# Kernel tuning notes

Measured on AMD Instinct MI355X. Metric: run time of the kernel, lower is better.

Reference implementation:

```python
import jax, jax.numpy as jnp
import numpy as np

EMB = 512
HEADS = 8
KEY_DIM = 64


def setup_inputs() -> dict:
    key = jax.random.key(0)
    k1, k2, k3, k4, k5 = jax.random.split(key, 5)
    B, S = 4, 2048
    x = jax.random.normal(k1, (B, S, EMB), dtype=jnp.float32)
    keys = jax.random.normal(k2, (B, HEADS, S, KEY_DIM), dtype=jnp.float32)
    values = jax.random.normal(k3, (B, HEADS, S, KEY_DIM), dtype=jnp.float32)
    # torch.rand -> uniform [0,1)
    query_weights = jax.random.uniform(k4, (EMB, KEY_DIM * HEADS), dtype=jnp.float32)
    output_weights = jax.random.uniform(k5, (KEY_DIM * HEADS, EMB), dtype=jnp.float32)
    return {"x": x, "keys": keys, "values": values,
            "query_weights": query_weights, "output_weights": output_weights}


def reference(x, keys, values, query_weights, output_weights):
    B, S, _ = x.shape
    # Q projection: [B,S,E] @ [E,H*K] -> [B,H,S,K]
    q = (x @ query_weights).reshape(B, S, HEADS, KEY_DIM).transpose(0, 2, 1, 3)
    # scores: [B,H,S,S]
    scores = jnp.einsum('bhqk,bhsk->bhqs', q, keys) / jnp.sqrt(jnp.float32(KEY_DIM))
    attn = jax.nn.softmax(scores, axis=-1)
    # context: [B,H,S,K] -> [B,S,H*K]
    ctx = jnp.einsum('bhqs,bhsk->bhqk', attn, values)
    ctx = ctx.transpose(0, 2, 1, 3).reshape(B, S, HEADS * KEY_DIM)
    return ctx @ output_weights
```

## Files before the change

kernel.cpp:

```cpp
#include <hip/hip_runtime.h>
#include <hip/hip_bf16.h>

#define EMB 512
#define HEADS 8
#define KD 64
#define SEQ 2048
#define BATCH 4

typedef __attribute__((ext_vector_type(8))) short bf16x8;
typedef __attribute__((ext_vector_type(4))) float f32x4;

__device__ __forceinline__ unsigned short f2bf(float x) {
    union { float f; unsigned u; } v; v.f = x;
    unsigned r = v.u + 0x7fff + ((v.u >> 16) & 1);
    return (unsigned short)(r >> 16);
}
__device__ __forceinline__ float bf2f(unsigned short b) {
    union { unsigned u; float f; } v; v.u = ((unsigned)b) << 16;
    return v.f;
}
__device__ __forceinline__ unsigned pk2(float a, float b) {
    __hip_bfloat162 h = __float22bfloat162_rn(float2{a, b});
    unsigned u; __builtin_memcpy(&u, &h, 4); return u;
}

__global__ __launch_bounds__(256) void prep_all_kernel(
    const float* __restrict__ x,  const float* __restrict__ wq,
    const float* __restrict__ wo, const float* __restrict__ K,
    const float* __restrict__ V,
    unsigned short* __restrict__ ximg, unsigned short* __restrict__ wqimg,
    unsigned short* __restrict__ woimg, unsigned short* __restrict__ kimg,
    unsigned short* __restrict__ vimg) {
    const int bid = blockIdx.x;
    const int t   = threadIdx.x;

    if (bid < 1024) {
        const int rb = bid >> 3, ch = bid & 7;
        const float* src = x + (size_t)rb * 64 * EMB + ch * 64;
        unsigned short* dhi = ximg + (size_t)bid * 8192;
        unsigned short* dlo = dhi + 4096;
#pragma unroll
        for (int it = 0; it < 4; ++it) {
            const int idx = t + it * 256;
            const int row = idx >> 4, c4 = (idx & 15) << 2;
            const float4 v = *(const float4*)(src + (size_t)row * EMB + c4);
            const unsigned short h0 = f2bf(v.x), h1 = f2bf(v.y),
                                 h2 = f2bf(v.z), h3 = f2bf(v.w);
            *(uint2*)&dhi[row * 64 + c4] = make_uint2(
                (unsigned)h0 | ((unsigned)h1 << 16),
                (unsigned)h2 | ((unsigned)h3 << 16));
            *(uint2*)&dlo[row * 64 + c4] = make_uint2(
                (unsigned)f2bf(v.x - bf2f(h0)) | ((unsigned)f2bf(v.y - bf2f(h1)) << 16),
                (unsigned)f2bf(v.z - bf2f(h2)) | ((unsigned)f2bf(v.w - bf2f(h3)) << 16));
        }
    } else if (bid < 1152) {
        int widx = bid - 1024;
        const bool isq = widx < 64;
        if (!isq) widx -= 64;
        const int nb = widx >> 3, ch = widx & 7;
        const float* src = (isq ? wq : wo) + (size_t)(ch * 64) * EMB + nb * 64;
        unsigned short* dhi = isq ? (wqimg + (size_t)widx * 8192)
                                  : (woimg + (size_t)widx * 4096);
        unsigned short* dlo = dhi + 4096;
#pragma unroll
        for (int it = 0; it < 2; ++it) {
            const int idx = t + it * 256;
            const int sp  = idx & 31;
            const int c4  = (idx >> 5) << 2;
            const float* r0 = src + (size_t)(2 * sp) * EMB + c4;
            const float4 a = *(const float4*)r0;
            const float4 b = *(const float4*)(r0 + EMB);
#pragma unroll
            for (int j = 0; j < 4; ++j) {
                const float aj = (&a.x)[j], bj = (&b.x)[j];
                const unsigned short ah = f2bf(aj), bh = f2bf(bj);
                *(unsigned*)&dhi[(c4 + j) * 64 + 2 * sp] =
                    (unsigned)ah | ((unsigned)bh << 16);
                if (isq)
                    *(unsigned*)&dlo[(c4 + j) * 64 + 2 * sp] =
                        (unsigned)f2bf(aj - bf2f(ah)) | ((unsigned)f2bf(bj - bf2f(bh)) << 16);
            }
        }
    } else if (bid < 2176) {
        const int kt = bid - 1152;
        const float4* src = (const float4*)(K + (size_t)kt * 4096);
        unsigned short* dhi = kimg + (size_t)kt * 8192;
        unsigned short* dlo = dhi + 4096;
#pragma unroll
        for (int it = 0; it < 4; ++it) {
            const int idx = t + it * 256;
            const float4 v = src[idx];
            const unsigned short h0 = f2bf(v.x), h1 = f2bf(v.y),
                                 h2 = f2bf(v.z), h3 = f2bf(v.w);
            *(uint2*)&dhi[idx * 4] = make_uint2(
                (unsigned)h0 | ((unsigned)h1 << 16),
                (unsigned)h2 | ((unsigned)h3 << 16));
            *(uint2*)&dlo[idx * 4] = make_uint2(
                (unsigned)f2bf(v.x - bf2f(h0)) | ((unsigned)f2bf(v.y - bf2f(h1)) << 16),
                (unsigned)f2bf(v.z - bf2f(h2)) | ((unsigned)f2bf(v.w - bf2f(h3)) << 16));
        }
    } else {
        const int vt = bid - 2176;
        const float* src = V + (size_t)vt * 4096;
        unsigned short* dst = vimg + (size_t)vt * 4096;
#pragma unroll
        for (int it = 0; it < 2; ++it) {
            const int idx = t + it * 256;
            const int sp  = idx & 31;
            const int d4  = (idx >> 5) << 2;
            const float4 a = *(const float4*)(src + (2 * sp) * KD + d4);
            const float4 b = *(const float4*)(src + (2 * sp + 1) * KD + d4);
#pragma unroll
            for (int j = 0; j < 4; ++j) {
                *(unsigned*)&dst[(d4 + j) * 64 + 2 * sp] =
                    (unsigned)f2bf((&a.x)[j]) | ((unsigned)f2bf((&b.x)[j]) << 16);
            }
        }
    }
}

__global__ __launch_bounds__(256) void proj_q_kernel(
    const unsigned short* __restrict__ ximg,
    const unsigned short* __restrict__ wqimg,
    unsigned short* __restrict__ qhi_img,
    unsigned short* __restrict__ qlo_img) {
    __shared__ unsigned short x_s[2][64][72];
    __shared__ unsigned short w_t[2][64][72];

    const int t  = threadIdx.x;
    const int w  = t >> 6;
    const int l  = t & 63;
    const int g  = l >> 4;
    const int ln = l & 15;

    const int rb = blockIdx.x;
    const int nb = blockIdx.y;

    f32x4 acc[4];
#pragma unroll
    for (int cb = 0; cb < 4; ++cb) acc[cb] = (f32x4){0.f, 0.f, 0.f, 0.f};

    for (int ch = 0; ch < 8; ++ch) {
        __syncthreads();
        const uint4* xs = (const uint4*)(ximg + (size_t)(rb * 8 + ch) * 8192);
        const uint4* ws = (const uint4*)(wqimg + (size_t)(nb * 8 + ch) * 8192);
#pragma unroll
        for (int it = 0; it < 4; ++it) {
            const int idx = t + it * 256;
            const int hl  = idx >> 9;
            const int rem = idx & 511;
            *(uint4*)&x_s[hl][rem >> 3][(rem & 7) * 8] = xs[idx];
            *(uint4*)&w_t[hl][rem >> 3][(rem & 7) * 8] = ws[idx];
        }
        __syncthreads();

        bf16x8 ah[2], al[2];
#pragma unroll
        for (int kk = 0; kk < 2; ++kk) {
            ah[kk] = *(const bf16x8*)&x_s[0][w * 16 + ln][g * 8 + 32 * kk];
            al[kk] = *(const bf16x8*)&x_s[1][w * 16 + ln][g * 8 + 32 * kk];
        }
#pragma unroll
        for (int cb = 0; cb < 4; ++cb) {
            f32x4 c = acc[cb];
#pragma unroll
            for (int kk = 0; kk < 2; ++kk) {
                const bf16x8 bh = *(const bf16x8*)&w_t[0][cb * 16 + ln][g * 8 + 32 * kk];
                const bf16x8 bl = *(const bf16x8*)&w_t[1][cb * 16 + ln][g * 8 + 32 * kk];
                c = __builtin_amdgcn_mfma_f32_16x16x32_bf16(al[kk], bh, c, 0, 0, 0);
                c = __builtin_amdgcn_mfma_f32_16x16x32_bf16(ah[kk], bl, c, 0, 0, 0);
                c = __builtin_amdgcn_mfma_f32_16x16x32_bf16(ah[kk], bh, c, 0, 0, 0);
            }
            acc[cb] = c;
        }
    }

#pragma unroll
    for (int cb = 0; cb < 4; ++cb) {
#pragma unroll
        for (int r = 0; r < 4; ++r) {
            const int row = rb * 64 + w * 16 + 4 * g + r;
            const int k   = cb * 16 + ln;
            const float v = acc[cb][r] * 0.125f;
            const unsigned short hi = f2bf(v);
            const unsigned short lo = f2bf(v - bf2f(hi));
            const size_t off = ((size_t)((row >> 11) * HEADS + nb) * SEQ + (row & 2047)) * KD + k;
            qhi_img[off] = hi;
            qlo_img[off] = lo;
        }
    }
}

__global__ __launch_bounds__(256) void proj_o_kernel(
    const unsigned short* __restrict__ ctximg,
    const unsigned short* __restrict__ woimg,
    float* __restrict__ out) {
    __shared__ unsigned short x_s[64][72];
    __shared__ unsigned short w_t[64][72];

    const int t  = threadIdx.x;
    const int w  = t >> 6;
    const int l  = t & 63;
    const int g  = l >> 4;
    const int ln = l & 15;

    const int rb = blockIdx.x;
    const int nb = blockIdx.y;

    f32x4 acc[4];
#pragma unroll
    for (int cb = 0; cb < 4; ++cb) acc[cb] = (f32x4){0.f, 0.f, 0.f, 0.f};

    for (int ch = 0; ch < 8; ++ch) {
        __syncthreads();
        const uint4* xs = (const uint4*)(ctximg + (size_t)(rb * 8 + ch) * 4096);
        const uint4* ws = (const uint4*)(woimg + (size_t)(nb * 8 + ch) * 4096);
#pragma unroll
        for (int it = 0; it < 2; ++it) {
            const int idx = t + it * 256;
            *(uint4*)&x_s[idx >> 3][(idx & 7) * 8] = xs[idx];
            *(uint4*)&w_t[idx >> 3][(idx & 7) * 8] = ws[idx];
        }
        __syncthreads();

        bf16x8 ah[2];
#pragma unroll
        for (int kk = 0; kk < 2; ++kk)
            ah[kk] = *(const bf16x8*)&x_s[w * 16 + ln][g * 8 + 32 * kk];
#pragma unroll
        for (int cb = 0; cb < 4; ++cb) {
            f32x4 c = acc[cb];
#pragma unroll
            for (int kk = 0; kk < 2; ++kk) {
                const bf16x8 bh = *(const bf16x8*)&w_t[cb * 16 + ln][g * 8 + 32 * kk];
                c = __builtin_amdgcn_mfma_f32_16x16x32_bf16(ah[kk], bh, c, 0, 0, 0);
            }
            acc[cb] = c;
        }
    }

#pragma unroll
    for (int cb = 0; cb < 4; ++cb) {
#pragma unroll
        for (int r = 0; r < 4; ++r) {
            const int row = rb * 64 + w * 16 + 4 * g + r;
            const int col = nb * 64 + cb * 16 + ln;
            out[(size_t)row * EMB + col] = acc[cb][r];
        }
    }
}

__global__ __launch_bounds__(256) void attn4_kernel(
    const unsigned short* __restrict__ qhi_img,
    const unsigned short* __restrict__ qlo_img,
    const unsigned short* __restrict__ kimg,
    const unsigned short* __restrict__ vimg,
    unsigned short* __restrict__ ctximg) {
    constexpr int NT  = 64;
    constexpr int LDK = 72;

    __shared__ unsigned short k_s[2][NT][LDK];
    __shared__ unsigned short v_t[KD][LDK];
    __shared__ unsigned short p_s[4][16][LDK];

    const int t  = threadIdx.x;
    const int w  = t >> 6;
    const int l  = t & 63;
    const int g  = l >> 4;
    const int ln = l & 15;

    const int bh = blockIdx.y;
    const int q0 = blockIdx.x * 64 + w * 16;

    bf16x8 qhi[2], qlo[2];
    {
        const size_t qoff = ((size_t)bh * SEQ + q0 + ln) * KD;
#pragma unroll
        for (int kk = 0; kk < 2; ++kk) {
            qhi[kk] = *(const bf16x8*)&qhi_img[qoff + g * 8 + 32 * kk];
            qlo[kk] = *(const bf16x8*)&qlo_img[qoff + g * 8 + 32 * kk];
        }
    }

    f32x4 acc[4];
#pragma unroll
    for (int db = 0; db < 4; ++db) acc[db] = (f32x4){0.f, 0.f, 0.f, 0.f};
    float m_run = -1e30f, l_run = 0.0f;

    for (int tile = 0; tile < SEQ / NT; ++tile) {
        __syncthreads();

        const uint4* ksrc = (const uint4*)(kimg + (size_t)(bh * 32 + tile) * 8192);
#pragma unroll
        for (int it = 0; it < 4; ++it) {
            const int idx = t + it * 256;
            const int hl  = idx >> 9;
            const int rem = idx & 511;
            *(uint4*)&k_s[hl][rem >> 3][(rem & 7) * 8] = ksrc[idx];
        }
        const uint4* vsrc = (const uint4*)(vimg + (size_t)(bh * 32 + tile) * 4096);
#pragma unroll
        for (int it = 0; it < 2; ++it) {
            const int idx = t + it * 256;
            *(uint4*)&v_t[idx >> 3][(idx & 7) * 8] = vsrc[idx];
        }
        __syncthreads();

        f32x4 st[4];
#pragma unroll
        for (int sb = 0; sb < 4; ++sb) {
            f32x4 c = (f32x4){0.f, 0.f, 0.f, 0.f};
#pragma unroll
            for (int kk = 0; kk < 2; ++kk) {
                const bf16x8 khi = *(const bf16x8*)&k_s[0][sb * 16 + ln][g * 8 + 32 * kk];
                const bf16x8 klo = *(const bf16x8*)&k_s[1][sb * 16 + ln][g * 8 + 32 * kk];
                c = __builtin_amdgcn_mfma_f32_16x16x32_bf16(klo, qhi[kk], c, 0, 0, 0);
                c = __builtin_amdgcn_mfma_f32_16x16x32_bf16(khi, qlo[kk], c, 0, 0, 0);
                c = __builtin_amdgcn_mfma_f32_16x16x32_bf16(khi, qhi[kk], c, 0, 0, 0);
            }
            st[sb] = c;
        }

        float tm = st[0][0];
#pragma unroll
        for (int sb = 0; sb < 4; ++sb)
#pragma unroll
            for (int r = 0; r < 4; ++r) tm = fmaxf(tm, st[sb][r]);
        tm = fmaxf(tm, __shfl_xor(tm, 16));
        tm = fmaxf(tm, __shfl_xor(tm, 32));

        const float m_new  = fmaxf(m_run, tm);
        const float scalef = __expf(m_run - m_new);
        m_run = m_new;

        float rs = 0.f;
#pragma unroll
        for (int sb = 0; sb < 4; ++sb) {
            const float p0 = __expf(st[sb][0] - m_new);
            const float p1 = __expf(st[sb][1] - m_new);
            const float p2 = __expf(st[sb][2] - m_new);
            const float p3 = __expf(st[sb][3] - m_new);
            rs += (p0 + p1) + (p2 + p3);
            *(uint2*)&p_s[w][ln][sb * 16 + g * 4] =
                make_uint2(pk2(p0, p1), pk2(p2, p3));
        }
        rs += __shfl_xor(rs, 16);
        rs += __shfl_xor(rs, 32);
        l_run = l_run * scalef + rs;

#pragma unroll
        for (int r = 0; r < 4; ++r) {
            const float sr = __shfl(scalef, 4 * g + r);
#pragma unroll
            for (int db = 0; db < 4; ++db) acc[db][r] *= sr;
        }

        bf16x8 pa[2];
#pragma unroll
        for (int kk = 0; kk < 2; ++kk)
            pa[kk] = *(const bf16x8*)&p_s[w][ln][g * 8 + 32 * kk];
#pragma unroll
        for (int db = 0; db < 4; ++db) {
            f32x4 c = acc[db];
#pragma unroll
            for (int kk = 0; kk < 2; ++kk) {
                const bf16x8 vb = *(const bf16x8*)&v_t[ln + 16 * db][g * 8 + 32 * kk];
                c = __builtin_amdgcn_mfma_f32_16x16x32_bf16(pa[kk], vb, c, 0, 0, 0);
            }
            acc[db] = c;
        }
    }

    const float invl = 1.0f / l_run;
    const int rb  = (bh >> 3) * 32 + blockIdx.x;
    const int chh = bh & 7;
    unsigned short* cbase = ctximg + ((size_t)rb * 8 + chh) * 4096;
#pragma unroll
    for (int r = 0; r < 4; ++r) {
        const float iv = __shfl(invl, 4 * g + r);
        const int row = w * 16 + 4 * g + r;
#pragma unroll
        for (int db = 0; db < 4; ++db)
            cbase[row * 64 + db * 16 + ln] = f2bf(acc[db][r] * iv);
    }
}

__global__ __launch_bounds__(256) void prep_k_kernel(const float* __restrict__ K,
                                                     unsigned short* __restrict__ kimg) {
    const int bt = blockIdx.x;
    const float4* src = (const float4*)(K + (size_t)bt * 4096);
    unsigned short* dhi = kimg + (size_t)bt * 8192;
    unsigned short* dlo = dhi + 4096;
#pragma unroll
    for (int it = 0; it < 4; ++it) {
        const int idx = threadIdx.x + it * 256;
        const float4 v = src[idx];
        const unsigned short h0 = f2bf(v.x), h1 = f2bf(v.y),
                             h2 = f2bf(v.z), h3 = f2bf(v.w);
        *(uint2*)&dhi[idx * 4] = make_uint2(
            (unsigned)h0 | ((unsigned)h1 << 16),
            (unsigned)h2 | ((unsigned)h3 << 16));
        *(uint2*)&dlo[idx * 4] = make_uint2(
            (unsigned)f2bf(v.x - bf2f(h0)) | ((unsigned)f2bf(v.y - bf2f(h1)) << 16),
            (unsigned)f2bf(v.z - bf2f(h2)) | ((unsigned)f2bf(v.w - bf2f(h3)) << 16));
    }
}

__global__ __launch_bounds__(256) void prep_v_kernel(const float* __restrict__ V,
                                                     unsigned short* __restrict__ vimg) {
    const int bt = blockIdx.x;
    const float* src = V + (size_t)bt * 4096;
    unsigned short* dst = vimg + (size_t)bt * 4096;
#pragma unroll
    for (int it = 0; it < 2; ++it) {
        const int idx = threadIdx.x + it * 256;
        const int sp  = idx & 31;
        const int d4  = (idx >> 5) << 2;
        const float4 a = *(const float4*)(src + (2 * sp) * KD + d4);
        const float4 b = *(const float4*)(src + (2 * sp + 1) * KD + d4);
#pragma unroll
        for (int j = 0; j < 4; ++j) {
            *(unsigned*)&dst[(d4 + j) * 64 + 2 * sp] =
                (unsigned)f2bf((&a.x)[j]) | ((unsigned)f2bf((&b.x)[j]) << 16);
        }
    }
}

template <int PREP>
__global__ __launch_bounds__(256) void attn3_kernel(const float* __restrict__ Q,
                                                    const float* __restrict__ Keys,
                                                    const float* __restrict__ Vals,
                                                    const unsigned short* __restrict__ kimg,
                                                    const unsigned short* __restrict__ vimg,
                                                    float* __restrict__ out) {
    constexpr int NT  = 64;
    constexpr int LDK = 72;

    __shared__ unsigned short k_s[2][NT][LDK];
    __shared__ unsigned short v_t[KD][LDK];
    __shared__ unsigned short p_s[4][16][LDK];

    const int t  = threadIdx.x;
    const int w  = t >> 6;
    const int l  = t & 63;
    const int g  = l >> 4;
    const int ln = l & 15;

    const int bh = blockIdx.y;
    const int q0 = blockIdx.x * 64 + w * 16;

    const float* kbase = Keys + (size_t)bh * SEQ * KD;
    const float* vbase = Vals + (size_t)bh * SEQ * KD;
    const float* qptr  = Q + ((size_t)bh * SEQ + q0 + ln) * KD;

    bf16x8 qhi[2], qlo[2];
#pragma unroll
    for (int kk = 0; kk < 2; ++kk) {
        const float* p = qptr + g * 8 + 32 * kk;
#pragma unroll
        for (int j = 0; j < 8; ++j) {
            const float xv = p[j] * 0.125f;
            const unsigned short h = f2bf(xv);
            qhi[kk][j] = (short)h;
            qlo[kk][j] = (short)f2bf(xv - bf2f(h));
        }
    }

    f32x4 acc[4];
#pragma unroll
    for (int db = 0; db < 4; ++db) acc[db] = (f32x4){0.f, 0.f, 0.f, 0.f};
    float m_run = -1e30f, l_run = 0.0f;

    for (int tile = 0; tile < SEQ / NT; ++tile) {
        __syncthreads();

        if (PREP) {
            const uint4* ksrc = (const uint4*)(kimg + (size_t)(bh * 32 + tile) * 8192);
#pragma unroll
            for (int it = 0; it < 4; ++it) {
                const int idx = t + it * 256;
                const int hl  = idx >> 9;
                const int rem = idx & 511;
                *(uint4*)&k_s[hl][rem >> 3][(rem & 7) * 8] = ksrc[idx];
            }
            const uint4* vsrc = (const uint4*)(vimg + (size_t)(bh * 32 + tile) * 4096);
#pragma unroll
            for (int it = 0; it < 2; ++it) {
                const int idx = t + it * 256;
                *(uint4*)&v_t[idx >> 3][(idx & 7) * 8] = vsrc[idx];
            }
        } else {
            const float* kt = kbase + (size_t)tile * NT * KD;
            const float* vt = vbase + (size_t)tile * NT * KD;
#pragma unroll
            for (int it = 0; it < 4; ++it) {
                const int idx = t + it * 256;
                const int s   = idx >> 4;
                const int d4  = (idx & 15) << 2;
                const float4 kv = *(const float4*)(kt + s * KD + d4);
                unsigned short h0 = f2bf(kv.x), h1 = f2bf(kv.y),
                               h2 = f2bf(kv.z), h3 = f2bf(kv.w);
                *(uint2*)&k_s[0][s][d4] = make_uint2(
                    (unsigned)h0 | ((unsigned)h1 << 16),
                    (unsigned)h2 | ((unsigned)h3 << 16));
                *(uint2*)&k_s[1][s][d4] = make_uint2(
                    (unsigned)f2bf(kv.x - bf2f(h0)) | ((unsigned)f2bf(kv.y - bf2f(h1)) << 16),
                    (unsigned)f2bf(kv.z - bf2f(h2)) | ((unsigned)f2bf(kv.w - bf2f(h3)) << 16));
            }
#pragma unroll
            for (int it = 0; it < 2; ++it) {
                const int idx = t + it * 256;
                const int sp  = idx & 31;
                const int d4  = (idx >> 5) << 2;
                const float* v0 = vt + (2 * sp) * KD + d4;
                const float4 a = *(const float4*)v0;
                const float4 b = *(const float4*)(v0 + KD);
#pragma unroll
                for (int j = 0; j < 4; ++j) {
                    *(unsigned*)&v_t[d4 + j][2 * sp] =
                        (unsigned)f2bf((&a.x)[j]) | ((unsigned)f2bf((&b.x)[j]) << 16);
                }
            }
        }
        __syncthreads();

        f32x4 st[4];
#pragma unroll
        for (int sb = 0; sb < 4; ++sb) {
            f32x4 c = (f32x4){0.f, 0.f, 0.f, 0.f};
#pragma unroll
            for (int kk = 0; kk < 2; ++kk) {
                const bf16x8 khi = *(const bf16x8*)&k_s[0][sb * 16 + ln][g * 8 + 32 * kk];
                const bf16x8 klo = *(const bf16x8*)&k_s[1][sb * 16 + ln][g * 8 + 32 * kk];
                c = __builtin_amdgcn_mfma_f32_16x16x32_bf16(klo, qhi[kk], c, 0, 0, 0);
                c = __builtin_amdgcn_mfma_f32_16x16x32_bf16(khi, qlo[kk], c, 0, 0, 0);
                c = __builtin_amdgcn_mfma_f32_16x16x32_bf16(khi, qhi[kk], c, 0, 0, 0);
            }
            st[sb] = c;
        }

        float tm = st[0][0];
#pragma unroll
        for (int sb = 0; sb < 4; ++sb)
#pragma unroll
            for (int r = 0; r < 4; ++r) tm = fmaxf(tm, st[sb][r]);
        tm = fmaxf(tm, __shfl_xor(tm, 16));
        tm = fmaxf(tm, __shfl_xor(tm, 32));

        const float m_new  = fmaxf(m_run, tm);
        const float scalef = __expf(m_run - m_new);
        m_run = m_new;

        float rs = 0.f;
#pragma unroll
        for (int sb = 0; sb < 4; ++sb) {
            const float p0 = __expf(st[sb][0] - m_new);
            const float p1 = __expf(st[sb][1] - m_new);
            const float p2 = __expf(st[sb][2] - m_new);
            const float p3 = __expf(st[sb][3] - m_new);
            rs += (p0 + p1) + (p2 + p3);
            *(uint2*)&p_s[w][ln][sb * 16 + g * 4] =
                make_uint2(pk2(p0, p1), pk2(p2, p3));
        }
        rs += __shfl_xor(rs, 16);
        rs += __shfl_xor(rs, 32);
        l_run = l_run * scalef + rs;

#pragma unroll
        for (int r = 0; r < 4; ++r) {
            const float sr = __shfl(scalef, 4 * g + r);
#pragma unroll
            for (int db = 0; db < 4; ++db) acc[db][r] *= sr;
        }

        bf16x8 pa[2];
#pragma unroll
        for (int kk = 0; kk < 2; ++kk)
            pa[kk] = *(const bf16x8*)&p_s[w][ln][g * 8 + 32 * kk];
#pragma unroll
        for (int db = 0; db < 4; ++db) {
            f32x4 c = acc[db];
#pragma unroll
            for (int kk = 0; kk < 2; ++kk) {
                const bf16x8 vb = *(const bf16x8*)&v_t[ln + 16 * db][g * 8 + 32 * kk];
                c = __builtin_amdgcn_mfma_f32_16x16x32_bf16(pa[kk], vb, c, 0, 0, 0);
            }
            acc[db] = c;
        }
    }

    const float invl = 1.0f / l_run;
    const int b = bh >> 3, h = bh & 7;
#pragma unroll
    for (int r = 0; r < 4; ++r) {
        const float iv = __shfl(invl, 4 * g + r);
        float* orow = out + ((size_t)(b * SEQ + q0 + 4 * g + r) * EMB) + h * KD + ln;
#pragma unroll
        for (int db = 0; db < 4; ++db) orow[16 * db] = acc[db][r] * iv;
    }
}

template <int TRANSQ>
__global__ __launch_bounds__(256) void proj_mfma_kernel(const float* __restrict__ in,
                                                        const float* __restrict__ W,
                                                        float* __restrict__ out) {
    __shared__ unsigned short x_s[2][64][72];
    __shared__ unsigned short w_t[2][64][72];

    const int t  = threadIdx.x;
    const int w  = t >> 6;
    const int l  = t & 63;
    const int g  = l >> 4;
    const int ln = l & 15;

    const int row0 = blockIdx.x * 64;
    const int n0   = blockIdx.y * 64;

    f32x4 acc[4];
#pragma unroll
    for (int cb = 0; cb < 4; ++cb) acc[cb] = (f32x4){0.f, 0.f, 0.f, 0.f};

    for (int ch = 0; ch < EMB / 64; ++ch) {
        __syncthreads();
#pragma unroll
        for (int it = 0; it < 4; ++it) {
            const int idx = t + it * 256;
            const int s   = idx >> 4;
            const int d4  = (idx & 15) << 2;
            const float4 xv = *(const float4*)(in + (size_t)(row0 + s) * EMB + ch * 64 + d4);
            const unsigned short h0 = f2bf(xv.x), h1 = f2bf(xv.y),
                                 h2 = f2bf(xv.z), h3 = f2bf(xv.w);
            *(uint2*)&x_s[0][s][d4] = make_uint2(
                (unsigned)h0 | ((unsigned)h1 << 16),
                (unsigned)h2 | ((unsigned)h3 << 16));
            *(uint2*)&x_s[1][s][d4] = make_uint2(
                (unsigned)f2bf(xv.x - bf2f(h0)) | ((unsigned)f2bf(xv.y - bf2f(h1)) << 16),
                (unsigned)f2bf(xv.z - bf2f(h2)) | ((unsigned)f2bf(xv.w - bf2f(h3)) << 16));
        }
#pragma unroll
        for (int it = 0; it < 2; ++it) {
            const int idx = t + it * 256;
            const int sp  = idx & 31;
            const int c4  = (idx >> 5) << 2;
            const float* wrow = W + (size_t)(ch * 64 + 2 * sp) * EMB + n0 + c4;
            const float4 a = *(const float4*)wrow;
            const float4 b = *(const float4*)(wrow + EMB);
#pragma unroll
            for (int j = 0; j < 4; ++j) {
                const float aj = (&a.x)[j], bj = (&b.x)[j];
                const unsigned short ah = f2bf(aj), bh = f2bf(bj);
                *(unsigned*)&w_t[0][c4 + j][2 * sp] =
                    (unsigned)ah | ((unsigned)bh << 16);
                *(unsigned*)&w_t[1][c4 + j][2 * sp] =
                    (unsigned)f2bf(aj - bf2f(ah)) | ((unsigned)f2bf(bj - bf2f(bh)) << 16);
            }
        }
        __syncthreads();

        bf16x8 ah[2], al[2];
#pragma unroll
        for (int kk = 0; kk < 2; ++kk) {
            ah[kk] = *(const bf16x8*)&x_s[0][w * 16 + ln][g * 8 + 32 * kk];
            al[kk] = *(const bf16x8*)&x_s[1][w * 16 + ln][g * 8 + 32 * kk];
        }
#pragma unroll
        for (int cb = 0; cb < 4; ++cb) {
            f32x4 c = acc[cb];
#pragma unroll
            for (int kk = 0; kk < 2; ++kk) {
                const bf16x8 bh = *(const bf16x8*)&w_t[0][cb * 16 + ln][g * 8 + 32 * kk];
                const bf16x8 bl = *(const bf16x8*)&w_t[1][cb * 16 + ln][g * 8 + 32 * kk];
                c = __builtin_amdgcn_mfma_f32_16x16x32_bf16(al[kk], bh, c, 0, 0, 0);
                c = __builtin_amdgcn_mfma_f32_16x16x32_bf16(ah[kk], bl, c, 0, 0, 0);
                c = __builtin_amdgcn_mfma_f32_16x16x32_bf16(ah[kk], bh, c, 0, 0, 0);
            }
            acc[cb] = c;
        }
    }

#pragma unroll
    for (int cb = 0; cb < 4; ++cb) {
#pragma unroll
        for (int r = 0; r < 4; ++r) {
            const int row = row0 + w * 16 + 4 * g + r;
            const int col = n0 + cb * 16 + ln;
            if (TRANSQ) {
                const int b = row >> 11, s = row & 2047;
                const int h = col >> 6, k = col & 63;
                out[((size_t)(b * HEADS + h) * SEQ + s) * KD + k] = acc[cb][r];
            } else {
                out[(size_t)row * EMB + col] = acc[cb][r];
            }
        }
    }
}

__global__ __launch_bounds__(256) void proj_fp32_kernel(const float* __restrict__ in,
                                                        const float* __restrict__ W,
                                                        float* __restrict__ out) {
    __shared__ float x_s[8][EMB];
    const int block_row = blockIdx.x * 8;

    const float4* in4 = (const float4*)(in + (size_t)block_row * EMB);
    float4* xs4 = (float4*)(&x_s[0][0]);
    for (int i = threadIdx.x; i < 8 * EMB / 4; i += 256) xs4[i] = in4[i];
    __syncthreads();

    const int n  = (threadIdx.x & 127) * 4;
    const int rg = threadIdx.x >> 7;

    float acc[4][4] = {};
    for (int e = 0; e < EMB; ++e) {
        const float4 w4 = *(const float4*)(W + (size_t)e * EMB + n);
#pragma unroll
        for (int rr = 0; rr < 4; ++rr) {
            const float xv = x_s[rg + rr * 2][e];
            acc[rr][0] += xv * w4.x;
            acc[rr][1] += xv * w4.y;
            acc[rr][2] += xv * w4.z;
            acc[rr][3] += xv * w4.w;
        }
    }
#pragma unroll
    for (int rr = 0; rr < 4; ++rr) {
        const int row = block_row + rg + rr * 2;
        float4 o;
        o.x = acc[rr][0]; o.y = acc[rr][1]; o.z = acc[rr][2]; o.w = acc[rr][3];
        *(float4*)(out + (size_t)row * EMB + n) = o;
    }
}

extern "C" void kernel_launch(void* const* d_in, const int* in_sizes, int n_in,
                              void* d_out, int out_size, void* d_ws, size_t ws_size,
                              hipStream_t stream) {
    const float* x  = (const float*)d_in[0];
    const float* ks = (const float*)d_in[1];
    const float* vs = (const float*)d_in[2];
    const float* wq = (const float*)d_in[3];
    const float* wo = (const float*)d_in[4];
    float* out = (float*)d_out;

    const int M = BATCH * SEQ;

    const size_t XIMG_OFF = 0;
    const size_t WQ_OFF   = 16777216;
    const size_t WO_OFF   = 17825792;
    const size_t KIMG_OFF = 18350080;
    const size_t VIMG_OFF = 35127296;
    const size_t QHI_OFF  = 43515904;
    const size_t QLO_OFF  = 51904512;
    const size_t CTX_OFF  = 60293120;
    const size_t TIER_A   = 68681728;

    if (ws_size >= TIER_A) {
        unsigned short* ximg  = (unsigned short*)((char*)d_ws + XIMG_OFF);
        unsigned short* wqimg = (unsigned short*)((char*)d_ws + WQ_OFF);
        unsigned short* woimg = (unsigned short*)((char*)d_ws + WO_OFF);
        unsigned short* kimg  = (unsigned short*)((char*)d_ws + KIMG_OFF);
        unsigned short* vimg  = (unsigned short*)((char*)d_ws + VIMG_OFF);
        unsigned short* qhi   = (unsigned short*)((char*)d_ws + QHI_OFF);
        unsigned short* qlo   = (unsigned short*)((char*)d_ws + QLO_OFF);
        unsigned short* ctx   = (unsigned short*)((char*)d_ws + CTX_OFF);

        prep_all_kernel<<<dim3(3200), dim3(256), 0, stream>>>(
            x, wq, wo, ks, vs, ximg, wqimg, woimg, kimg, vimg);
        proj_q_kernel<<<dim3(M / 64, HEADS), dim3(256), 0, stream>>>(ximg, wqimg, qhi, qlo);
        attn4_kernel<<<dim3(SEQ / 64, BATCH * HEADS), dim3(256), 0, stream>>>(
            qhi, qlo, kimg, vimg, ctx);
        proj_o_kernel<<<dim3(M / 64, EMB / 64), dim3(256), 0, stream>>>(ctx, woimg, out);
        return;
    }

    const size_t QBYTES  = (size_t)BATCH * HEADS * SEQ * KD * 4;
    const size_t CBYTES  = (size_t)BATCH * SEQ * EMB * 4;
    const size_t KIBYTES = (size_t)BATCH * HEADS * SEQ * KD * 2 * 2;
    const size_t VIBYTES = (size_t)BATCH * HEADS * SEQ * KD * 2;

    float* Q = (float*)d_ws;
    const bool mid_ws  = ws_size >= QBYTES + CBYTES;
    const bool full_ws = ws_size >= QBYTES + CBYTES + KIBYTES + VIBYTES;
    float* ctxf = mid_ws ? (float*)((char*)d_ws + QBYTES) : out;
    unsigned short* kimg = (unsigned short*)((char*)d_ws + QBYTES + CBYTES);
    unsigned short* vimg = (unsigned short*)((char*)d_ws + QBYTES + CBYTES + KIBYTES);

    proj_mfma_kernel<1><<<dim3(M / 64, EMB / 64), dim3(256), 0, stream>>>(x, wq, Q);

    if (full_ws) {
        prep_k_kernel<<<dim3(BATCH * HEADS * 32), dim3(256), 0, stream>>>(ks, kimg);
        prep_v_kernel<<<dim3(BATCH * HEADS * 32), dim3(256), 0, stream>>>(vs, vimg);
        attn3_kernel<1><<<dim3(SEQ / 64, BATCH * HEADS), dim3(256), 0, stream>>>(
            Q, ks, vs, kimg, vimg, ctxf);
    } else {
        attn3_kernel<0><<<dim3(SEQ / 64, BATCH * HEADS), dim3(256), 0, stream>>>(
            Q, ks, vs, nullptr, nullptr, ctxf);
    }

    if (mid_ws) {
        proj_mfma_kernel<0><<<dim3(M / 64, EMB / 64), dim3(256), 0, stream>>>(ctxf, wo, out);
    } else {
        proj_fp32_kernel<<<dim3(M / 8), dim3(256), 0, stream>>>(ctxf, wo, out);
    }
}
```

Measured before the change: 245.3 us.

## Rewrite attention with 32x32 MFMA tiles, split-KV waves, and lazy rescaling

```diff
diff --git a/kernel.cpp b/kernel.cpp
--- a/kernel.cpp
+++ b/kernel.cpp
@@ -9,6 +9,7 @@
 
 typedef __attribute__((ext_vector_type(8))) short bf16x8;
 typedef __attribute__((ext_vector_type(4))) float f32x4;
+typedef __attribute__((ext_vector_type(16))) float f32x16;
 
 __device__ __forceinline__ unsigned short f2bf(float x) {
     union { float f; unsigned u; } v; v.f = x;
@@ -250,44 +251,47 @@
     }
 }
 
-__global__ __launch_bounds__(256) void attn4_kernel(
+__global__ __launch_bounds__(256) void attn5_kernel(
     const unsigned short* __restrict__ qhi_img,
     const unsigned short* __restrict__ qlo_img,
     const unsigned short* __restrict__ kimg,
     const unsigned short* __restrict__ vimg,
     unsigned short* __restrict__ ctximg) {
-    constexpr int NT  = 64;
     constexpr int LDK = 72;
-
-    __shared__ unsigned short k_s[2][NT][LDK];
-    __shared__ unsigned short v_t[KD][LDK];
-    __shared__ unsigned short p_s[4][16][LDK];
-
-    const int t  = threadIdx.x;
-    const int w  = t >> 6;
-    const int l  = t & 63;
-    const int g  = l >> 4;
-    const int ln = l & 15;
+    constexpr int LDP = 40;
+
+    __shared__ unsigned short k_s[2][64][LDK];
+    __shared__ unsigned short v_t[64][LDK];
+    __shared__ unsigned short p_s[4][32][LDP];
+    __shared__ float m_arr[2][2][32], l_arr[2][2][32];
+
+    const int t   = threadIdx.x;
+    const int w   = t >> 6;
+    const int l   = t & 63;
+    const int qh  = w >> 1;
+    const int sh  = w & 1;
+    const int q32 = l & 31;
+    const int h   = l >> 5;
 
     const int bh = blockIdx.y;
-    const int q0 = blockIdx.x * 64 + w * 16;
-
-    bf16x8 qhi[2], qlo[2];
+    const int q0 = blockIdx.x * 64;
+
+    bf16x8 qhi[4], qlo[4];
     {
-        const size_t qoff = ((size_t)bh * SEQ + q0 + ln) * KD;
-#pragma unroll
-        for (int kk = 0; kk < 2; ++kk) {
-            qhi[kk] = *(const bf16x8*)&qhi_img[qoff + g * 8 + 32 * kk];
-            qlo[kk] = *(const bf16x8*)&qlo_img[qoff + g * 8 + 32 * kk];
-        }
-    }
-
-    f32x4 acc[4];
-#pragma unroll
-    for (int db = 0; db < 4; ++db) acc[db] = (f32x4){0.f, 0.f, 0.f, 0.f};
-    float m_run = -1e30f, l_run = 0.0f;
-
-    for (int tile = 0; tile < SEQ / NT; ++tile) {
+        const size_t qoff = ((size_t)bh * SEQ + q0 + qh * 32 + q32) * KD + 8 * h;
+#pragma unroll
+        for (int ks = 0; ks < 4; ++ks) {
+            qhi[ks] = *(const bf16x8*)&qhi_img[qoff + 16 * ks];
+            qlo[ks] = *(const bf16x8*)&qlo_img[qoff + 16 * ks];
+        }
+    }
+
+    f32x16 acc0, acc1;
+#pragma unroll
+    for (int i = 0; i < 16; ++i) { acc0[i] = 0.f; acc1[i] = 0.f; }
+    float m_run = -1e30f, l_run = 0.f;
+
+    for (int tile = 0; tile < SEQ / 64; ++tile) {
         __syncthreads();
 
         const uint4* ksrc = (const uint4*)(kimg + (size_t)(bh * 32 + tile) * 8192);
@@ -306,82 +310,93 @@
         }
         __syncthreads();
 
-        f32x4 st[4];
-#pragma unroll
-        for (int sb = 0; sb < 4; ++sb) {
-            f32x4 c = (f32x4){0.f, 0.f, 0.f, 0.f};
-#pragma unroll
-            for (int kk = 0; kk < 2; ++kk) {
-                const bf16x8 khi = *(const bf16x8*)&k_s[0][sb * 16 + ln][g * 8 + 32 * kk];
-                const bf16x8 klo = *(const bf16x8*)&k_s[1][sb * 16 + ln][g * 8 + 32 * kk];
-                c = __builtin_amdgcn_mfma_f32_16x16x32_bf16(klo, qhi[kk], c, 0, 0, 0);
-                c = __builtin_amdgcn_mfma_f32_16x16x32_bf16(khi, qlo[kk], c, 0, 0, 0);
-                c = __builtin_amdgcn_mfma_f32_16x16x32_bf16(khi, qhi[kk], c, 0, 0, 0);
-            }
-            st[sb] = c;
-        }
-
-        float tm = st[0][0];
-#pragma unroll
-        for (int sb = 0; sb < 4; ++sb)
-#pragma unroll
-            for (int r = 0; r < 4; ++r) tm = fmaxf(tm, st[sb][r]);
-        tm = fmaxf(tm, __shfl_xor(tm, 16));
+        f32x16 st;
+#pragma unroll
+        for (int i = 0; i < 16; ++i) st[i] = 0.f;
+        const int srow = sh * 32 + q32;
+#pragma unroll
+        for (int ks = 0; ks < 4; ++ks) {
+            const bf16x8 khi = *(const bf16x8*)&k_s[0][srow][16 * ks + 8 * h];
+            const bf16x8 klo = *(const bf16x8*)&k_s[1][srow][16 * ks + 8 * h];
+            st = __builtin_amdgcn_mfma_f32_32x32x16_bf16(klo, qhi[ks], st, 0, 0, 0);
+            st = __builtin_amdgcn_mfma_f32_32x32x16_bf16(khi, qlo[ks], st, 0, 0, 0);
+            st = __builtin_amdgcn_mfma_f32_32x32x16_bf16(khi, qhi[ks], st, 0, 0, 0);
+        }
+
+        float tm = st[0];
+#pragma unroll
+        for (int i = 1; i < 16; ++i) tm = fmaxf(tm, st[i]);
         tm = fmaxf(tm, __shfl_xor(tm, 32));
 
-        const float m_new  = fmaxf(m_run, tm);
-        const float scalef = __expf(m_run - m_new);
-        m_run = m_new;
+        if (__any(tm > m_run + 8.0f)) {
+            const float m_new = fmaxf(m_run, tm);
+            const float sc = __expf(m_run - m_new);
+            m_run = m_new;
+            l_run *= sc;
+#pragma unroll
+            for (int r = 0; r < 16; ++r) {
+                const int qrow = (r & 3) + 8 * (r >> 2) + 4 * h;
+                const float sr = __shfl(sc, qrow);
+                acc0[r] *= sr; acc1[r] *= sr;
+            }
+        }
 
         float rs = 0.f;
 #pragma unroll
-        for (int sb = 0; sb < 4; ++sb) {
-            const float p0 = __expf(st[sb][0] - m_new);
-            const float p1 = __expf(st[sb][1] - m_new);
-            const float p2 = __expf(st[sb][2] - m_new);
-            const float p3 = __expf(st[sb][3] - m_new);
-            rs += (p0 + p1) + (p2 + p3);
-            *(uint2*)&p_s[w][ln][sb * 16 + g * 4] =
-                make_uint2(pk2(p0, p1), pk2(p2, p3));
-        }
-        rs += __shfl_xor(rs, 16);
+        for (int i = 0; i < 8; ++i) {
+            const float pa_ = __expf(st[2 * i]     - m_run);
+            const float pb_ = __expf(st[2 * i + 1] - m_run);
+            rs += pa_ + pb_;
+            const int sbase = ((2 * i) & 3) + 8 * (i >> 1) + 4 * h;
+            *(unsigned*)&p_s[w][q32][sbase] = pk2(pa_, pb_);
+        }
         rs += __shfl_xor(rs, 32);
-        l_run = l_run * scalef + rs;
-
-#pragma unroll
-        for (int r = 0; r < 4; ++r) {
-            const float sr = __shfl(scalef, 4 * g + r);
-#pragma unroll
-            for (int db = 0; db < 4; ++db) acc[db][r] *= sr;
-        }
-
-        bf16x8 pa[2];
-#pragma unroll
-        for (int kk = 0; kk < 2; ++kk)
-            pa[kk] = *(const bf16x8*)&p_s[w][ln][g * 8 + 32 * kk];
-#pragma unroll
-        for (int db = 0; db < 4; ++db) {
-            f32x4 c = acc[db];
-#pragma unroll
-            for (int kk = 0; kk < 2; ++kk) {
-                const bf16x8 vb = *(const bf16x8*)&v_t[ln + 16 * db][g * 8 + 32 * kk];
-                c = __builtin_amdgcn_mfma_f32_16x16x32_bf16(pa[kk], vb, c, 0, 0, 0);
-            }
-            acc[db] = c;
-        }
-    }
-
-    const float invl = 1.0f / l_run;
-    const int rb  = (bh >> 3) * 32 + blockIdx.x;
-    const int chh = bh & 7;
-    unsigned short* cbase = ctximg + ((size_t)rb * 8 + chh) * 4096;
-#pragma unroll
-    for (int r = 0; r < 4; ++r) {
-        const float iv = __shfl(invl, 4 * g + r);
-        const int row = w * 16 + 4 * g + r;
-#pragma unroll
-        for (int db = 0; db < 4; ++db)
-            cbase[row * 64 + db * 16 + ln] = f2bf(acc[db][r] * iv);
+        l_run += rs;
+
+#pragma unroll
+        for (int ks = 0; ks < 2; ++ks) {
+            const bf16x8 pa = *(const bf16x8*)&p_s[w][q32][16 * ks + 8 * h];
+            const bf16x8 v0 = *(const bf16x8*)&v_t[q32]     [sh * 32 + 16 * ks + 8 * h];
+            const bf16x8 v1 = *(const bf16x8*)&v_t[32 + q32][sh * 32 + 16 * ks + 8 * h];
+            acc0 = __builtin_amdgcn_mfma_f32_32x32x16_bf16(pa, v0, acc0, 0, 0, 0);
+            acc1 = __builtin_amdgcn_mfma_f32_32x32x16_bf16(pa, v1, acc1, 0, 0, 0);
+        }
+    }
+
+    __syncthreads();
+    if (l < 32) { m_arr[sh][qh][l] = m_run; l_arr[sh][qh][l] = l_run; }
+    __syncthreads();
+    const float m_o = m_arr[sh ^ 1][qh][q32];
+    const float l_o = l_arr[sh ^ 1][qh][q32];
+    const float m_f = fmaxf(m_run, m_o);
+    const float a_own = __expf(m_run - m_f);
+    const float inv_lf = 1.0f / (a_own * l_run + __expf(m_o - m_f) * l_o);
+
+    float* cmerge = (float*)&k_s[0][0][0];
+    if (sh == 1) {
+#pragma unroll
+        for (int r = 0; r < 16; ++r) {
+            const int qrow = (r & 3) + 8 * (r >> 2) + 4 * h;
+            const float sr = __shfl(a_own, qrow);
+            cmerge[(qh * 32 + qrow) * 64 + q32]      = acc0[r] * sr;
+            cmerge[(qh * 32 + qrow) * 64 + 32 + q32] = acc1[r] * sr;
+        }
+    }
+    __syncthreads();
+    if (sh == 0) {
+        const int rb  = (bh >> 3) * 32 + blockIdx.x;
+        const int chh = bh & 7;
+        unsigned short* cbase = ctximg + ((size_t)rb * 8 + chh) * 4096;
+#pragma unroll
+        for (int r = 0; r < 16; ++r) {
+            const int qrow = (r & 3) + 8 * (r >> 2) + 4 * h;
+            const float sr  = __shfl(a_own, qrow);
+            const float ivr = __shfl(inv_lf, qrow);
+            const float v0 = (acc0[r] * sr + cmerge[(qh * 32 + qrow) * 64 + q32]) * ivr;
+            const float v1 = (acc1[r] * sr + cmerge[(qh * 32 + qrow) * 64 + 32 + q32]) * ivr;
+            cbase[(qh * 32 + qrow) * 64 + q32]      = f2bf(v0);
+            cbase[(qh * 32 + qrow) * 64 + 32 + q32] = f2bf(v1);
+        }
     }
 }
 
@@ -765,7 +780,7 @@
         prep_all_kernel<<<dim3(3200), dim3(256), 0, stream>>>(
             x, wq, wo, ks, vs, ximg, wqimg, woimg, kimg, vimg);
         proj_q_kernel<<<dim3(M / 64, HEADS), dim3(256), 0, stream>>>(ximg, wqimg, qhi, qlo);
-        attn4_kernel<<<dim3(SEQ / 64, BATCH * HEADS), dim3(256), 0, stream>>>(
+        attn5_kernel<<<dim3(SEQ / 64, BATCH * HEADS), dim3(256), 0, stream>>>(
             qhi, qlo, kimg, vimg, ctx);
         proj_o_kernel<<<dim3(M / 64, EMB / 64), dim3(256), 0, stream>>>(ctx, woimg, out);
         return;
```

New measurement: 243.2 us. No clear change (-0.8%).
